# Kernel optimization log

Measured on AMD Instinct MI355X. Metric: run time of the kernel, lower is better.

The kernel has to match this reference:

```python
import jax, jax.numpy as jnp
import numpy as np

H = 64      # num query heads
HKV = 8     # num key/value heads
D = 64      # head_dim
HID = 2880  # hidden_size
B = 8       # batch (num sequences)
Q = 16      # query tokens per sequence
P = 128     # kv pages per sequence
PAGE = 16   # kv page size
NPAGES = 2048  # total pages in cache pool
NEG = -1e9  # finite stand-in for -inf mask (avoids inf arithmetic; exp underflows to 0 identically)


def setup_inputs() -> dict:
    key = jax.random.key(0)
    ks = jax.random.split(key, 6)
    n = B * Q
    S = P * PAGE
    hidden_states = jax.random.normal(ks[0], (n, HID), jnp.float32) * 0.02
    kv_cache_at_layer = jax.random.normal(ks[1], (NPAGES, 2, PAGE, HKV, D), jnp.float32)
    qkv_dim = D * (H + 2 * HKV)
    w_qkv = jax.random.normal(ks[2], (qkv_dim, HID), jnp.float32) * 0.02
    b_qkv = jnp.zeros((qkv_dim,), jnp.float32)
    w_o = jax.random.normal(ks[3], (HID, H * D), jnp.float32) * 0.02
    b_o = jnp.zeros((HID,), jnp.float32)
    sinks = jax.random.normal(ks[4], (H,), jnp.float32)
    qo_indptr = (jnp.arange(B + 1) * Q).astype(jnp.int32)
    kv_page_indptr = (jnp.arange(B + 1) * P).astype(jnp.int32)
    kv_last_page_lens = jnp.full((B,), PAGE, jnp.int32)
    kv_page_indices = jnp.asarray(np.random.default_rng(0).permutation(NPAGES)[:B * P], jnp.int32)
    # causal mask: query i of each sequence sits at absolute position S - Q + i
    qpos = S - Q + jnp.arange(Q)
    mask = jnp.where(jnp.arange(S)[None, :] <= qpos[:, None], 0.0, NEG).astype(jnp.float32)
    attention_mask = jnp.broadcast_to(mask[None], (B, Q, S)).reshape(-1)
    return dict(hidden_states=hidden_states, kv_cache_at_layer=kv_cache_at_layer,
                attention_mask=attention_mask, w_qkv=w_qkv, b_qkv=b_qkv, w_o=w_o, b_o=b_o,
                sinks=sinks, qo_indptr=qo_indptr, kv_page_indptr=kv_page_indptr,
                kv_last_page_lens=kv_last_page_lens, kv_page_indices=kv_page_indices)


def reference(hidden_states, kv_cache_at_layer, attention_mask, w_qkv, b_qkv, w_o, b_o,
              sinks, qo_indptr, kv_page_indptr, kv_last_page_lens, kv_page_indices):
    n = hidden_states.shape[0]
    b = qo_indptr.shape[0] - 1
    q_len = n // b                              # uniform ragged layout (see setup)
    p = kv_page_indices.shape[0] // b
    page = kv_cache_at_layer.shape[2]
    s = p * page
    g = H // HKV                                # query heads per kv head (GQA groups)
    scaling = D ** -0.5

    qkv = hidden_states @ w_qkv.T + b_qkv                       # [n, (H+2*HKV)*D]
    q = qkv[:, :H * D].reshape(b, q_len, HKV, g, D) * scaling    # [b q hkv g d]

    pages = kv_page_indices.reshape(b, p)
    k = kv_cache_at_layer[pages, 0].reshape(b, s, HKV, D)        # gather pages -> [b s hkv d]
    v = kv_cache_at_layer[pages, 1].reshape(b, s, HKV, D)

    scores = jnp.einsum('bqhgd,bshd->bhgqs', q, k).astype(jnp.float32)
    mask = attention_mask.reshape(b, q_len, s)
    # keys beyond the valid portion of the last page are invalid
    valid = jnp.arange(s)[None, :] < ((p - 1) * page + kv_last_page_lens[:, None])
    mask = jnp.where(valid[:, None, :], mask, NEG)
    scores = scores + mask[:, None, None, :, :]

    # online-softmax merge across pages is equivalent to this single pass;
    # running max starts at 0 in the original, hence the clamp to 0
    m = jnp.maximum(scores.max(axis=-1), 0.0)                    # [b hkv g q]
    pexp = jnp.exp(scores - m[..., None])                        # [b hkv g q s]
    sink = sinks.reshape(HKV, g).astype(jnp.float32)
    sum_exp = pexp.sum(axis=-1) + jnp.exp(sink[None, :, :, None] - m)
    num = jnp.einsum('bhgqs,bshd->bhgqd', pexp, v.astype(jnp.float32))
    attn = num / sum_exp[..., None]                              # [b hkv g q d]
    attn = attn.transpose(0, 3, 1, 2, 4).reshape(n, H * D)       # q (h d)
    return attn.astype(hidden_states.dtype) @ w_o.T + b_o
```

## Files before the change

### kernel.cpp

```cpp
#include <hip/hip_runtime.h>
#include <hip/hip_bf16.h>

#define BB      8
#define QL      16
#define NHKV    8
#define NG      8
#define DD      64
#define HIDN    2880
#define PP      128
#define PGSZ    16
#define SS      2048
#define NQ      4096
#define NSPLIT  8
#define KSQ     5
#define KCQ     576
#define KSO     8
#define KCO     512

typedef short bf16x8 __attribute__((ext_vector_type(8)));
typedef short short4v __attribute__((ext_vector_type(4)));
typedef float f32x4  __attribute__((ext_vector_type(4)));

__device__ inline short f2bf(float f) {
  __hip_bfloat16 h = __float2bfloat16(f);
  union { __hip_bfloat16 h; short s; } u; u.h = h;
  return u.s;
}

__device__ inline float bf2f(short s) {
  union { float f; unsigned u; } u;
  u.u = ((unsigned)(unsigned short)s) << 16;
  return u.f;
}

__device__ inline bf16x8 cvt8(float4 a, float4 b) {
  bf16x8 r;
  r[0] = f2bf(a.x); r[1] = f2bf(a.y); r[2] = f2bf(a.z); r[3] = f2bf(a.w);
  r[4] = f2bf(b.x); r[5] = f2bf(b.y); r[6] = f2bf(b.z); r[7] = f2bf(b.w);
  return r;
}

__device__ inline bf16x8 pack8(const float* __restrict__ p) {
  float4 a = *(const float4*)p;
  float4 b = *(const float4*)(p + 4);
  return cvt8(a, b);
}

__global__ __launch_bounds__(256) void k_qkv_split(const float* __restrict__ hid,
                                                   const float* __restrict__ wq,
                                                   short* __restrict__ qpart) {
  const int n0 = blockIdx.x * 32;
  const int ks = blockIdx.y;
  const int tid = threadIdx.x;
  const int wid = tid >> 6, lane = tid & 63;
  const int lo = lane & 15, hi = lane >> 4;
  const int m0 = wid * 32;

  const float* xr0 = hid + (size_t)(m0 + lo) * HIDN;
  const float* xr1 = hid + (size_t)(m0 + 16 + lo) * HIDN;
  const float* wr0 = wq + (size_t)(n0 + lo) * HIDN;
  const float* wr1 = wq + (size_t)(n0 + 16 + lo) * HIDN;
  const int kb = ks * KCQ + hi * 8;

  f32x4 acc[2][2];
#pragma unroll
  for (int mt = 0; mt < 2; ++mt)
#pragma unroll
    for (int nt = 0; nt < 2; ++nt) acc[mt][nt] = (f32x4){0.f, 0.f, 0.f, 0.f};

  float4 bufA[4][2], bufB[4][2];
#define LOADQ(dst, kk) { \
    dst[0][0] = *(const float4*)(xr0 + (kk)); dst[0][1] = *(const float4*)(xr0 + (kk) + 4); \
    dst[1][0] = *(const float4*)(xr1 + (kk)); dst[1][1] = *(const float4*)(xr1 + (kk) + 4); \
    dst[2][0] = *(const float4*)(wr0 + (kk)); dst[2][1] = *(const float4*)(wr0 + (kk) + 4); \
    dst[3][0] = *(const float4*)(wr1 + (kk)); dst[3][1] = *(const float4*)(wr1 + (kk) + 4); }
#define MFMAQ(buf) { \
    bf16x8 a0 = cvt8(buf[0][0], buf[0][1]); \
    bf16x8 a1 = cvt8(buf[1][0], buf[1][1]); \
    bf16x8 w0 = cvt8(buf[2][0], buf[2][1]); \
    bf16x8 w1 = cvt8(buf[3][0], buf[3][1]); \
    acc[0][0] = __builtin_amdgcn_mfma_f32_16x16x32_bf16(a0, w0, acc[0][0], 0, 0, 0); \
    acc[0][1] = __builtin_amdgcn_mfma_f32_16x16x32_bf16(a0, w1, acc[0][1], 0, 0, 0); \
    acc[1][0] = __builtin_amdgcn_mfma_f32_16x16x32_bf16(a1, w0, acc[1][0], 0, 0, 0); \
    acc[1][1] = __builtin_amdgcn_mfma_f32_16x16x32_bf16(a1, w1, acc[1][1], 0, 0, 0); }

  LOADQ(bufA, kb);
#pragma unroll
  for (int it = 0; it < 9; ++it) {
    const int kk = kb + it * 64;
    LOADQ(bufB, kk + 32);
    MFMAQ(bufA);
    if (it < 8) LOADQ(bufA, kk + 64);
    MFMAQ(bufB);
  }
#undef LOADQ
#undef MFMAQ

  short* qp = qpart + (size_t)ks * 128 * NQ;
#pragma unroll
  for (int mt = 0; mt < 2; ++mt)
#pragma unroll
    for (int nt = 0; nt < 2; ++nt)
#pragma unroll
      for (int r = 0; r < 4; ++r) {
        int m = m0 + mt * 16 + hi * 4 + r;
        int n = n0 + nt * 16 + lo;
        qp[(size_t)m * NQ + n] = f2bf(acc[mt][nt][r]);
      }
}

__global__ __launch_bounds__(256) void k_attn(const float* __restrict__ kvc,
                                              const int* __restrict__ pidx,
                                              const int* __restrict__ llen,
                                              const short* __restrict__ qpart,
                                              const float* __restrict__ bq,
                                              short* __restrict__ opart,
                                              float* __restrict__ lbuf) {
  const int blk = blockIdx.x;
  const int pair = blk >> 3, split = blk & 7;
  const int b = pair >> 3, kvh = pair & 7;
  const int tid = threadIdx.x;
  const int wid = tid >> 6, lane = tid & 63;
  const int lo = lane & 15, hi = lane >> 4;
  const int wrow = wid * 32;

  __shared__ short plds[128][72];
  __shared__ float vlds[64][65];

  bf16x8 qf[2][2];
#pragma unroll
  for (int mt = 0; mt < 2; ++mt) {
    int r = wrow + mt * 16 + lo;
    int g = r >> 4, qq = r & 15;
    int m = b * QL + qq;
    int h = kvh * NG + g;
#pragma unroll
    for (int kg = 0; kg < 2; ++kg) {
      int n = h * DD + kg * 32 + hi * 8;
      float4 bb0 = *(const float4*)(bq + n);
      float4 bb1 = *(const float4*)(bq + n + 4);
      float s[8];
      s[0] = bb0.x; s[1] = bb0.y; s[2] = bb0.z; s[3] = bb0.w;
      s[4] = bb1.x; s[5] = bb1.y; s[6] = bb1.z; s[7] = bb1.w;
#pragma unroll
      for (int k2 = 0; k2 < KSQ; ++k2) {
        bf16x8 p = *(const bf16x8*)(qpart + ((size_t)k2 * 128 + m) * NQ + n);
#pragma unroll
        for (int j = 0; j < 8; ++j) s[j] += bf2f(p[j]);
      }
      bf16x8 q8;
#pragma unroll
      for (int j = 0; j < 8; ++j) q8[j] = f2bf(s[j] * 0.125f);
      qf[mt][kg] = q8;
    }
  }

  float l_part[2][4];
  f32x4 o_acc[2][4];
#pragma unroll
  for (int mt = 0; mt < 2; ++mt)
#pragma unroll
    for (int j = 0; j < 4; ++j) l_part[mt][j] = 0.f;
#pragma unroll
  for (int mt = 0; mt < 2; ++mt)
#pragma unroll
    for (int dt = 0; dt < 4; ++dt) o_acc[mt][dt] = (f32x4){0.f, 0.f, 0.f, 0.f};

  const int sKeepEnd = (PP - 1) * PGSZ + llen[b];
  const int* pib = pidx + b * PP;
  const int sBeg = split * (SS / NSPLIT);
  const int sEnd = sBeg + (SS / NSPLIT);

  for (int s0 = sBeg; s0 < sEnd; s0 += 64) {
    const int p0 = s0 >> 4;

    float4 vreg[4];
    const int vsr = tid >> 4;
    const int vc4 = (tid & 15) * 4;
#pragma unroll
    for (int pc = 0; pc < 4; ++pc) {
      int pg = pib[p0 + pc];
      vreg[pc] = *(const float4*)(kvc +
          ((((size_t)pg * 2 + 1) * PGSZ + vsr) * NHKV + kvh) * DD + vc4);
    }

    f32x4 sc[2][4];
#pragma unroll
    for (int mt = 0; mt < 2; ++mt)
#pragma unroll
      for (int nt = 0; nt < 4; ++nt) sc[mt][nt] = (f32x4){0.f, 0.f, 0.f, 0.f};

#pragma unroll
    for (int nt = 0; nt < 4; ++nt) {
      int pg = pib[p0 + nt];
      const float* kp = kvc + ((((size_t)pg * 2 + 0) * PGSZ + lo) * NHKV + kvh) * DD;
#pragma unroll
      for (int kg = 0; kg < 2; ++kg) {
        bf16x8 kf = pack8(kp + kg * 32 + hi * 8);
        sc[0][nt] = __builtin_amdgcn_mfma_f32_16x16x32_bf16(qf[0][kg], kf, sc[0][nt], 0, 0, 0);
        sc[1][nt] = __builtin_amdgcn_mfma_f32_16x16x32_bf16(qf[1][kg], kf, sc[1][nt], 0, 0, 0);
      }
    }

    if (s0 + 64 > SS - QL) {
#pragma unroll
      for (int mt = 0; mt < 2; ++mt)
#pragma unroll
        for (int j = 0; j < 4; ++j) {
          int r = wrow + mt * 16 + hi * 4 + j;
          int qq = r & 15;
          int sLimQ = (SS - QL) + qq;
#pragma unroll
          for (int nt = 0; nt < 4; ++nt) {
            int s = s0 + nt * 16 + lo;
            bool keep = (s <= sLimQ) && (s < sKeepEnd);
            sc[mt][nt][j] = keep ? sc[mt][nt][j] : -1.0e9f;
          }
        }
    }

#pragma unroll
    for (int mt = 0; mt < 2; ++mt)
#pragma unroll
      for (int j = 0; j < 4; ++j)
#pragma unroll
        for (int nt = 0; nt < 4; ++nt) {
          float p = __expf(sc[mt][nt][j]);
          sc[mt][nt][j] = p;
          l_part[mt][j] += p;
        }

    __syncthreads();
#pragma unroll
    for (int pc = 0; pc < 4; ++pc) {
      int sl = pc * 16 + vsr;
      vlds[sl][vc4]     = vreg[pc].x;
      vlds[sl][vc4 + 1] = vreg[pc].y;
      vlds[sl][vc4 + 2] = vreg[pc].z;
      vlds[sl][vc4 + 3] = vreg[pc].w;
    }
#pragma unroll
    for (int mt = 0; mt < 2; ++mt)
#pragma unroll
      for (int j = 0; j < 4; ++j) {
        int r = wrow + mt * 16 + hi * 4 + j;
#pragma unroll
        for (int nt = 0; nt < 4; ++nt)
          plds[r][nt * 16 + lo] = f2bf(sc[mt][nt][j]);
      }
    __syncthreads();

#pragma unroll
    for (int kg = 0; kg < 2; ++kg) {
      bf16x8 pa[2];
      pa[0] = *(const bf16x8*)(&plds[wrow + lo][kg * 32 + hi * 8]);
      pa[1] = *(const bf16x8*)(&plds[wrow + 16 + lo][kg * 32 + hi * 8]);
#pragma unroll
      for (int dt = 0; dt < 4; ++dt) {
        bf16x8 vf;
#pragma unroll
        for (int j = 0; j < 8; ++j)
          vf[j] = f2bf(vlds[kg * 32 + hi * 8 + j][dt * 16 + lo]);
        o_acc[0][dt] = __builtin_amdgcn_mfma_f32_16x16x32_bf16(pa[0], vf, o_acc[0][dt], 0, 0, 0);
        o_acc[1][dt] = __builtin_amdgcn_mfma_f32_16x16x32_bf16(pa[1], vf, o_acc[1][dt], 0, 0, 0);
      }
    }
  }

#pragma unroll
  for (int mt = 0; mt < 2; ++mt)
#pragma unroll
    for (int j = 0; j < 4; ++j)
#pragma unroll
      for (int off = 1; off < 16; off <<= 1)
        l_part[mt][j] += __shfl_xor(l_part[mt][j], off, 64);

  short* op = opart + (size_t)(pair * NSPLIT + split) * 128 * DD;
#pragma unroll
  for (int mt = 0; mt < 2; ++mt)
#pragma unroll
    for (int dt = 0; dt < 4; ++dt)
#pragma unroll
      for (int j = 0; j < 4; ++j) {
        int r = wrow + mt * 16 + hi * 4 + j;
        op[r * DD + dt * 16 + lo] = f2bf(o_acc[mt][dt][j]);
      }
  if (lo == 0) {
#pragma unroll
    for (int mt = 0; mt < 2; ++mt)
#pragma unroll
      for (int j = 0; j < 4; ++j) {
        int r = wrow + mt * 16 + hi * 4 + j;
        lbuf[(size_t)(pair * NSPLIT + split) * 128 + r] = l_part[mt][j];
      }
  }
}

__global__ __launch_bounds__(256) void k_merge(const short* __restrict__ opart,
                                               const float* __restrict__ lbuf,
                                               const float* __restrict__ sinks,
                                               short* __restrict__ attnbf) {
  const int pair = blockIdx.x;
  const int b = pair >> 3, kvh = pair & 7;
  const int tid = threadIdx.x;

  __shared__ float Ls[128];
  if (tid < 128) {
    int r = tid, g = r >> 4;
    float L = __expf(sinks[kvh * NG + g]);
#pragma unroll
    for (int s2 = 0; s2 < NSPLIT; ++s2)
      L += lbuf[(size_t)(pair * NSPLIT + s2) * 128 + r];
    Ls[r] = L;
  }
  __syncthreads();

  for (int u = tid; u < 128 * 16; u += 256) {
    int r = u >> 4, c4 = (u & 15) * 4;
    float o0 = 0.f, o1 = 0.f, o2 = 0.f, o3 = 0.f;
#pragma unroll
    for (int s2 = 0; s2 < NSPLIT; ++s2) {
      short4v pv = *(const short4v*)(opart +
          ((size_t)(pair * NSPLIT + s2) * 128 + r) * DD + c4);
      o0 += bf2f(pv[0]); o1 += bf2f(pv[1]); o2 += bf2f(pv[2]); o3 += bf2f(pv[3]);
    }
    float inv = 1.0f / Ls[r];
    int g = r >> 4, qq = r & 15;
    int h = kvh * NG + g;
    short4v ov;
    ov[0] = f2bf(o0 * inv); ov[1] = f2bf(o1 * inv);
    ov[2] = f2bf(o2 * inv); ov[3] = f2bf(o3 * inv);
    *(short4v*)(attnbf + (size_t)(b * QL + qq) * NQ + h * DD + c4) = ov;
  }
}

__global__ __launch_bounds__(256) void k_out_split(const short* __restrict__ attnbf,
                                                   const float* __restrict__ wo,
                                                   short* __restrict__ outpart) {
  const int n0 = blockIdx.x * 32;
  const int ks = blockIdx.y;
  const int tid = threadIdx.x;
  const int wid = tid >> 6, lane = tid & 63;
  const int lo = lane & 15, hi = lane >> 4;
  const int m0 = wid * 32;

  const short* ar0 = attnbf + (size_t)(m0 + lo) * NQ;
  const short* ar1 = attnbf + (size_t)(m0 + 16 + lo) * NQ;
  const float* wr0 = wo + (size_t)(n0 + lo) * NQ;
  const float* wr1 = wo + (size_t)(n0 + 16 + lo) * NQ;
  const int kb = ks * KCO + hi * 8;

  f32x4 acc[2][2];
#pragma unroll
  for (int mt = 0; mt < 2; ++mt)
#pragma unroll
    for (int nt = 0; nt < 2; ++nt) acc[mt][nt] = (f32x4){0.f, 0.f, 0.f, 0.f};

  bf16x8 aA[2], aB[2];
  float4 wA[2][2], wB[2][2];
#define LOADO(adst, wdst, kk) { \
    adst[0] = *(const bf16x8*)(ar0 + (kk)); \
    adst[1] = *(const bf16x8*)(ar1 + (kk)); \
    wdst[0][0] = *(const float4*)(wr0 + (kk)); wdst[0][1] = *(const float4*)(wr0 + (kk) + 4); \
    wdst[1][0] = *(const float4*)(wr1 + (kk)); wdst[1][1] = *(const float4*)(wr1 + (kk) + 4); }
#define MFMAO(abuf, wbuf) { \
    bf16x8 ww0 = cvt8(wbuf[0][0], wbuf[0][1]); \
    bf16x8 ww1 = cvt8(wbuf[1][0], wbuf[1][1]); \
    acc[0][0] = __builtin_amdgcn_mfma_f32_16x16x32_bf16(abuf[0], ww0, acc[0][0], 0, 0, 0); \
    acc[0][1] = __builtin_amdgcn_mfma_f32_16x16x32_bf16(abuf[0], ww1, acc[0][1], 0, 0, 0); \
    acc[1][0] = __builtin_amdgcn_mfma_f32_16x16x32_bf16(abuf[1], ww0, acc[1][0], 0, 0, 0); \
    acc[1][1] = __builtin_amdgcn_mfma_f32_16x16x32_bf16(abuf[1], ww1, acc[1][1], 0, 0, 0); }

  LOADO(aA, wA, kb);
#pragma unroll
  for (int it = 0; it < 8; ++it) {
    const int kk = kb + it * 64;
    LOADO(aB, wB, kk + 32);
    MFMAO(aA, wA);
    if (it < 7) LOADO(aA, wA, kk + 64);
    MFMAO(aB, wB);
  }
#undef LOADO
#undef MFMAO

  short* op = outpart + (size_t)ks * 128 * HIDN;
#pragma unroll
  for (int mt = 0; mt < 2; ++mt)
#pragma unroll
    for (int nt = 0; nt < 2; ++nt)
#pragma unroll
      for (int r = 0; r < 4; ++r) {
        int m = m0 + mt * 16 + hi * 4 + r;
        int n = n0 + nt * 16 + lo;
        op[(size_t)m * HIDN + n] = f2bf(acc[mt][nt][r]);
      }
}

__global__ __launch_bounds__(256) void k_ored(const short* __restrict__ outpart,
                                              const float* __restrict__ bo,
                                              float* __restrict__ out) {
  int idx = blockIdx.x * 256 + threadIdx.x;
  int m = idx / 720;
  int n = (idx - m * 720) * 4;
  float4 v = *(const float4*)(bo + n);
#pragma unroll
  for (int ks = 0; ks < KSO; ++ks) {
    short4v p = *(const short4v*)(outpart + ((size_t)ks * 128 + m) * HIDN + n);
    v.x += bf2f(p[0]); v.y += bf2f(p[1]); v.z += bf2f(p[2]); v.w += bf2f(p[3]);
  }
  *(float4*)(out + (size_t)m * HIDN + n) = v;
}

extern "C" void kernel_launch(void* const* d_in, const int* in_sizes, int n_in,
                              void* d_out, int out_size, void* d_ws, size_t ws_size,
                              hipStream_t stream) {
  const float* hid   = (const float*)d_in[0];
  const float* kvc   = (const float*)d_in[1];
  const float* wq    = (const float*)d_in[3];
  const float* bq    = (const float*)d_in[4];
  const float* wo    = (const float*)d_in[5];
  const float* bo    = (const float*)d_in[6];
  const float* sinks = (const float*)d_in[7];
  const int* llen    = (const int*)d_in[10];
  const int* pidx    = (const int*)d_in[11];
  float* out = (float*)d_out;

  char* ws = (char*)d_ws;
  short* qpart   = (short*)(ws + 0);
  short* attnbf  = (short*)(ws + 5242880);
  short* opart   = (short*)(ws + 6291456);
  float* lbuf    = (float*)(ws + 14680064);
  short* outpart = (short*)(ws + 14942208);

  k_qkv_split<<<dim3(128, KSQ), dim3(256), 0, stream>>>(hid, wq, qpart);
  k_attn<<<dim3(BB * NHKV * NSPLIT), dim3(256), 0, stream>>>(kvc, pidx, llen, qpart, bq, opart, lbuf);
  k_merge<<<dim3(BB * NHKV), dim3(256), 0, stream>>>(opart, lbuf, sinks, attnbf);
  k_out_split<<<dim3(HIDN / 32, KSO), dim3(256), 0, stream>>>(attnbf, wo, outpart);
  k_ored<<<dim3(360), dim3(256), 0, stream>>>(outpart, bo, out);
}
```

Before: 128.7 us.

## Software-pipeline K/V page loads in attention and split merge across more blocks

The attention loop is fully unrolled into four tiles with double-buffered V registers and K registers. The next tile's K and V page loads are issued right after the current QK MFMAs, so global latency overlaps with softmax and PV work. Page indices are preloaded into registers, and barriers use explicit lgkmcnt waits so pending global loads are not drained. The merge kernel is split four ways over head-dim columns to launch more blocks, at the cost of each block recomputing the row sums and higher register pressure in attention.

Result: slower. 134.3 us (+4.4%).

```diff
diff --git a/kernel.cpp b/kernel.cpp
--- a/kernel.cpp
+++ b/kernel.cpp
@@ -40,12 +40,6 @@
   return r;
 }
 
-__device__ inline bf16x8 pack8(const float* __restrict__ p) {
-  float4 a = *(const float4*)p;
-  float4 b = *(const float4*)(p + 4);
-  return cvt8(a, b);
-}
-
 __global__ __launch_bounds__(256) void k_qkv_split(const float* __restrict__ hid,
                                                    const float* __restrict__ wq,
                                                    short* __restrict__ qpart) {
@@ -169,103 +163,123 @@
   const int sKeepEnd = (PP - 1) * PGSZ + llen[b];
   const int* pib = pidx + b * PP;
   const int sBeg = split * (SS / NSPLIT);
-  const int sEnd = sBeg + (SS / NSPLIT);
-
-  for (int s0 = sBeg; s0 < sEnd; s0 += 64) {
-    const int p0 = s0 >> 4;
-
-    float4 vreg[4];
-    const int vsr = tid >> 4;
-    const int vc4 = (tid & 15) * 4;
-#pragma unroll
-    for (int pc = 0; pc < 4; ++pc) {
-      int pg = pib[p0 + pc];
-      vreg[pc] = *(const float4*)(kvc +
-          ((((size_t)pg * 2 + 1) * PGSZ + vsr) * NHKV + kvh) * DD + vc4);
-    }
-
-    f32x4 sc[2][4];
-#pragma unroll
-    for (int mt = 0; mt < 2; ++mt)
-#pragma unroll
-      for (int nt = 0; nt < 4; ++nt) sc[mt][nt] = (f32x4){0.f, 0.f, 0.f, 0.f};
-
-#pragma unroll
-    for (int nt = 0; nt < 4; ++nt) {
-      int pg = pib[p0 + nt];
-      const float* kp = kvc + ((((size_t)pg * 2 + 0) * PGSZ + lo) * NHKV + kvh) * DD;
-#pragma unroll
-      for (int kg = 0; kg < 2; ++kg) {
-        bf16x8 kf = pack8(kp + kg * 32 + hi * 8);
-        sc[0][nt] = __builtin_amdgcn_mfma_f32_16x16x32_bf16(qf[0][kg], kf, sc[0][nt], 0, 0, 0);
-        sc[1][nt] = __builtin_amdgcn_mfma_f32_16x16x32_bf16(qf[1][kg], kf, sc[1][nt], 0, 0, 0);
-      }
-    }
-
-    if (s0 + 64 > SS - QL) {
-#pragma unroll
-      for (int mt = 0; mt < 2; ++mt)
-#pragma unroll
-        for (int j = 0; j < 4; ++j) {
-          int r = wrow + mt * 16 + hi * 4 + j;
-          int qq = r & 15;
-          int sLimQ = (SS - QL) + qq;
-#pragma unroll
-          for (int nt = 0; nt < 4; ++nt) {
-            int s = s0 + nt * 16 + lo;
-            bool keep = (s <= sLimQ) && (s < sKeepEnd);
-            sc[mt][nt][j] = keep ? sc[mt][nt][j] : -1.0e9f;
-          }
-        }
-    }
-
-#pragma unroll
-    for (int mt = 0; mt < 2; ++mt)
-#pragma unroll
-      for (int j = 0; j < 4; ++j)
-#pragma unroll
-        for (int nt = 0; nt < 4; ++nt) {
-          float p = __expf(sc[mt][nt][j]);
-          sc[mt][nt][j] = p;
-          l_part[mt][j] += p;
-        }
-
-    __syncthreads();
-#pragma unroll
-    for (int pc = 0; pc < 4; ++pc) {
-      int sl = pc * 16 + vsr;
-      vlds[sl][vc4]     = vreg[pc].x;
-      vlds[sl][vc4 + 1] = vreg[pc].y;
-      vlds[sl][vc4 + 2] = vreg[pc].z;
-      vlds[sl][vc4 + 3] = vreg[pc].w;
-    }
-#pragma unroll
-    for (int mt = 0; mt < 2; ++mt)
-#pragma unroll
-      for (int j = 0; j < 4; ++j) {
-        int r = wrow + mt * 16 + hi * 4 + j;
-#pragma unroll
-        for (int nt = 0; nt < 4; ++nt)
-          plds[r][nt * 16 + lo] = f2bf(sc[mt][nt][j]);
-      }
-    __syncthreads();
-
-#pragma unroll
-    for (int kg = 0; kg < 2; ++kg) {
-      bf16x8 pa[2];
-      pa[0] = *(const bf16x8*)(&plds[wrow + lo][kg * 32 + hi * 8]);
-      pa[1] = *(const bf16x8*)(&plds[wrow + 16 + lo][kg * 32 + hi * 8]);
-#pragma unroll
-      for (int dt = 0; dt < 4; ++dt) {
-        bf16x8 vf;
-#pragma unroll
-        for (int j = 0; j < 8; ++j)
-          vf[j] = f2bf(vlds[kg * 32 + hi * 8 + j][dt * 16 + lo]);
-        o_acc[0][dt] = __builtin_amdgcn_mfma_f32_16x16x32_bf16(pa[0], vf, o_acc[0][dt], 0, 0, 0);
-        o_acc[1][dt] = __builtin_amdgcn_mfma_f32_16x16x32_bf16(pa[1], vf, o_acc[1][dt], 0, 0, 0);
-      }
-    }
-  }
+
+  const int vsr = tid >> 4;
+  const int vc4 = (tid & 15) * 4;
+
+  int pga[16];
+#pragma unroll
+  for (int i = 0; i < 16; ++i) pga[i] = pib[(sBeg >> 4) + i];
+
+  float4 kreg[4][4];
+  float4 vregA[4], vregB[4];
+
+#define KLOAD(NT, PG) { \
+    const float* kp_ = kvc + ((((size_t)(PG) * 2 + 0) * PGSZ + lo) * NHKV + kvh) * DD + hi * 8; \
+    kreg[NT][0] = *(const float4*)(kp_);      kreg[NT][1] = *(const float4*)(kp_ + 4); \
+    kreg[NT][2] = *(const float4*)(kp_ + 32); kreg[NT][3] = *(const float4*)(kp_ + 36); }
+#define VLOAD(DST, PC, PG) { \
+    DST[PC] = *(const float4*)(kvc + ((((size_t)(PG) * 2 + 1) * PGSZ + vsr) * NHKV + kvh) * DD + vc4); }
+#define BARX() { asm volatile("s_waitcnt lgkmcnt(0)" ::: "memory"); \
+    __builtin_amdgcn_s_barrier(); __builtin_amdgcn_sched_barrier(0); }
+
+#pragma unroll
+  for (int nt = 0; nt < 4; ++nt) KLOAD(nt, pga[nt]);
+#pragma unroll
+  for (int pc = 0; pc < 4; ++pc) VLOAD(vregA, pc, pga[pc]);
+
+#define TILE(S0, PI, VCUR, VNXT, PRE) { \
+    f32x4 sc[2][4]; \
+    _Pragma("unroll") \
+    for (int nt = 0; nt < 4; ++nt) { \
+      sc[0][nt] = (f32x4){0.f, 0.f, 0.f, 0.f}; \
+      sc[1][nt] = (f32x4){0.f, 0.f, 0.f, 0.f}; \
+    } \
+    _Pragma("unroll") \
+    for (int nt = 0; nt < 4; ++nt) { \
+      bf16x8 kf0 = cvt8(kreg[nt][0], kreg[nt][1]); \
+      bf16x8 kf1 = cvt8(kreg[nt][2], kreg[nt][3]); \
+      sc[0][nt] = __builtin_amdgcn_mfma_f32_16x16x32_bf16(qf[0][0], kf0, sc[0][nt], 0, 0, 0); \
+      sc[1][nt] = __builtin_amdgcn_mfma_f32_16x16x32_bf16(qf[1][0], kf0, sc[1][nt], 0, 0, 0); \
+      sc[0][nt] = __builtin_amdgcn_mfma_f32_16x16x32_bf16(qf[0][1], kf1, sc[0][nt], 0, 0, 0); \
+      sc[1][nt] = __builtin_amdgcn_mfma_f32_16x16x32_bf16(qf[1][1], kf1, sc[1][nt], 0, 0, 0); \
+    } \
+    if (PRE) { \
+      _Pragma("unroll") \
+      for (int nt = 0; nt < 4; ++nt) KLOAD(nt, pga[(PI) + 4 + nt]); \
+      _Pragma("unroll") \
+      for (int pc = 0; pc < 4; ++pc) VLOAD(VNXT, pc, pga[(PI) + 4 + pc]); \
+    } \
+    if ((S0) + 64 > SS - QL) { \
+      _Pragma("unroll") \
+      for (int mt = 0; mt < 2; ++mt) \
+        _Pragma("unroll") \
+        for (int j = 0; j < 4; ++j) { \
+          int r = wrow + mt * 16 + hi * 4 + j; \
+          int qq = r & 15; \
+          int sLimQ = (SS - QL) + qq; \
+          _Pragma("unroll") \
+          for (int nt = 0; nt < 4; ++nt) { \
+            int s = (S0) + nt * 16 + lo; \
+            bool keep = (s <= sLimQ) && (s < sKeepEnd); \
+            sc[mt][nt][j] = keep ? sc[mt][nt][j] : -1.0e9f; \
+          } \
+        } \
+    } \
+    _Pragma("unroll") \
+    for (int mt = 0; mt < 2; ++mt) \
+      _Pragma("unroll") \
+      for (int j = 0; j < 4; ++j) \
+        _Pragma("unroll") \
+        for (int nt = 0; nt < 4; ++nt) { \
+          float p = __expf(sc[mt][nt][j]); \
+          sc[mt][nt][j] = p; \
+          l_part[mt][j] += p; \
+        } \
+    BARX(); \
+    _Pragma("unroll") \
+    for (int pc = 0; pc < 4; ++pc) { \
+      int sl = pc * 16 + vsr; \
+      vlds[sl][vc4]     = VCUR[pc].x; \
+      vlds[sl][vc4 + 1] = VCUR[pc].y; \
+      vlds[sl][vc4 + 2] = VCUR[pc].z; \
+      vlds[sl][vc4 + 3] = VCUR[pc].w; \
+    } \
+    _Pragma("unroll") \
+    for (int mt = 0; mt < 2; ++mt) \
+      _Pragma("unroll") \
+      for (int j = 0; j < 4; ++j) { \
+        int r = wrow + mt * 16 + hi * 4 + j; \
+        _Pragma("unroll") \
+        for (int nt = 0; nt < 4; ++nt) \
+          plds[r][nt * 16 + lo] = f2bf(sc[mt][nt][j]); \
+      } \
+    BARX(); \
+    _Pragma("unroll") \
+    for (int kg = 0; kg < 2; ++kg) { \
+      bf16x8 pa0 = *(const bf16x8*)(&plds[wrow + lo][kg * 32 + hi * 8]); \
+      bf16x8 pa1 = *(const bf16x8*)(&plds[wrow + 16 + lo][kg * 32 + hi * 8]); \
+      _Pragma("unroll") \
+      for (int dt = 0; dt < 4; ++dt) { \
+        bf16x8 vf; \
+        _Pragma("unroll") \
+        for (int j = 0; j < 8; ++j) \
+          vf[j] = f2bf(vlds[kg * 32 + hi * 8 + j][dt * 16 + lo]); \
+        o_acc[0][dt] = __builtin_amdgcn_mfma_f32_16x16x32_bf16(pa0, vf, o_acc[0][dt], 0, 0, 0); \
+        o_acc[1][dt] = __builtin_amdgcn_mfma_f32_16x16x32_bf16(pa1, vf, o_acc[1][dt], 0, 0, 0); \
+      } \
+    } \
+  }
+
+  TILE(sBeg,       0,  vregA, vregB, 1)
+  TILE(sBeg + 64,  4,  vregB, vregA, 1)
+  TILE(sBeg + 128, 8,  vregA, vregB, 1)
+  TILE(sBeg + 192, 12, vregB, vregA, 0)
+
+#undef TILE
+#undef BARX
+#undef KLOAD
+#undef VLOAD
 
 #pragma unroll
   for (int mt = 0; mt < 2; ++mt)
@@ -300,7 +314,7 @@
                                                const float* __restrict__ lbuf,
                                                const float* __restrict__ sinks,
                                                short* __restrict__ attnbf) {
-  const int pair = blockIdx.x;
+  const int pair = blockIdx.x >> 2, quarter = blockIdx.x & 3;
   const int b = pair >> 3, kvh = pair & 7;
   const int tid = threadIdx.x;
 
@@ -315,8 +329,8 @@
   }
   __syncthreads();
 
-  for (int u = tid; u < 128 * 16; u += 256) {
-    int r = u >> 4, c4 = (u & 15) * 4;
+  for (int u = tid; u < 128 * 4; u += 256) {
+    int r = u >> 2, c4 = (quarter * 4 + (u & 3)) * 4;
     float o0 = 0.f, o1 = 0.f, o2 = 0.f, o3 = 0.f;
 #pragma unroll
     for (int s2 = 0; s2 < NSPLIT; ++s2) {
@@ -434,7 +448,7 @@
 
   k_qkv_split<<<dim3(128, KSQ), dim3(256), 0, stream>>>(hid, wq, qpart);
   k_attn<<<dim3(BB * NHKV * NSPLIT), dim3(256), 0, stream>>>(kvc, pidx, llen, qpart, bq, opart, lbuf);
-  k_merge<<<dim3(BB * NHKV), dim3(256), 0, stream>>>(opart, lbuf, sinks, attnbf);
+  k_merge<<<dim3(BB * NHKV * 4), dim3(256), 0, stream>>>(opart, lbuf, sinks, attnbf);
   k_out_split<<<dim3(HIDN / 32, KSO), dim3(256), 0, stream>>>(attnbf, wo, outpart);
   k_ored<<<dim3(360), dim3(256), 0, stream>>>(outpart, bo, out);
 }
```

## Fuse split-KV merge into output projection GEMM A-fragment loads

Applied to the files above, without the earlier changes.

Removes the separate merge kernel and instead reduces the per-split partial outputs and normalizes them by the softmax denominator while building A fragments inside the output projection kernel. Each block recomputes inverse denominators for its kv head into shared memory. This drops one launch and the intermediate attn buffer write/read. In exchange, each of the 90 n-blocks redundantly reads and sums all 8 split partials, multiplying opart traffic roughly 90-fold (mostly from L2) and adding ALU work to the GEMM inner loop.

New measurement: 198.0 us. +53.9%, slower.

```diff
diff --git a/kernel.cpp b/kernel.cpp
--- a/kernel.cpp
+++ b/kernel.cpp
@@ -296,45 +296,9 @@
   }
 }
 
-__global__ __launch_bounds__(256) void k_merge(const short* __restrict__ opart,
-                                               const float* __restrict__ lbuf,
-                                               const float* __restrict__ sinks,
-                                               short* __restrict__ attnbf) {
-  const int pair = blockIdx.x;
-  const int b = pair >> 3, kvh = pair & 7;
-  const int tid = threadIdx.x;
-
-  __shared__ float Ls[128];
-  if (tid < 128) {
-    int r = tid, g = r >> 4;
-    float L = __expf(sinks[kvh * NG + g]);
-#pragma unroll
-    for (int s2 = 0; s2 < NSPLIT; ++s2)
-      L += lbuf[(size_t)(pair * NSPLIT + s2) * 128 + r];
-    Ls[r] = L;
-  }
-  __syncthreads();
-
-  for (int u = tid; u < 128 * 16; u += 256) {
-    int r = u >> 4, c4 = (u & 15) * 4;
-    float o0 = 0.f, o1 = 0.f, o2 = 0.f, o3 = 0.f;
-#pragma unroll
-    for (int s2 = 0; s2 < NSPLIT; ++s2) {
-      short4v pv = *(const short4v*)(opart +
-          ((size_t)(pair * NSPLIT + s2) * 128 + r) * DD + c4);
-      o0 += bf2f(pv[0]); o1 += bf2f(pv[1]); o2 += bf2f(pv[2]); o3 += bf2f(pv[3]);
-    }
-    float inv = 1.0f / Ls[r];
-    int g = r >> 4, qq = r & 15;
-    int h = kvh * NG + g;
-    short4v ov;
-    ov[0] = f2bf(o0 * inv); ov[1] = f2bf(o1 * inv);
-    ov[2] = f2bf(o2 * inv); ov[3] = f2bf(o3 * inv);
-    *(short4v*)(attnbf + (size_t)(b * QL + qq) * NQ + h * DD + c4) = ov;
-  }
-}
-
-__global__ __launch_bounds__(256) void k_out_split(const short* __restrict__ attnbf,
+__global__ __launch_bounds__(256) void k_out_fused(const short* __restrict__ opart,
+                                                   const float* __restrict__ lbuf,
+                                                   const float* __restrict__ sinks,
                                                    const float* __restrict__ wo,
                                                    short* __restrict__ outpart) {
   const int n0 = blockIdx.x * 32;
@@ -344,8 +308,20 @@
   const int lo = lane & 15, hi = lane >> 4;
   const int m0 = wid * 32;
 
-  const short* ar0 = attnbf + (size_t)(m0 + lo) * NQ;
-  const short* ar1 = attnbf + (size_t)(m0 + 16 + lo) * NQ;
+  __shared__ float invLs[8][128];
+  for (int u = tid; u < 8 * 128; u += 256) {
+    int b = u >> 7, r = u & 127;
+    int g = r >> 4;
+    float L = __expf(sinks[ks * NG + g]);
+#pragma unroll
+    for (int s2 = 0; s2 < NSPLIT; ++s2)
+      L += lbuf[(size_t)((b * NHKV + ks) * NSPLIT + s2) * 128 + r];
+    invLs[b][r] = 1.0f / L;
+  }
+  __syncthreads();
+
+  const int b0 = (m0 >> 4), b1 = b0 + 1;
+  const int qq = lo;
   const float* wr0 = wo + (size_t)(n0 + lo) * NQ;
   const float* wr1 = wo + (size_t)(n0 + 16 + lo) * NQ;
   const int kb = ks * KCO + hi * 8;
@@ -356,31 +332,49 @@
 #pragma unroll
     for (int nt = 0; nt < 2; ++nt) acc[mt][nt] = (f32x4){0.f, 0.f, 0.f, 0.f};
 
-  bf16x8 aA[2], aB[2];
   float4 wA[2][2], wB[2][2];
-#define LOADO(adst, wdst, kk) { \
-    adst[0] = *(const bf16x8*)(ar0 + (kk)); \
-    adst[1] = *(const bf16x8*)(ar1 + (kk)); \
+#define WLOAD(wdst, kk) { \
     wdst[0][0] = *(const float4*)(wr0 + (kk)); wdst[0][1] = *(const float4*)(wr0 + (kk) + 4); \
     wdst[1][0] = *(const float4*)(wr1 + (kk)); wdst[1][1] = *(const float4*)(wr1 + (kk) + 4); }
-#define MFMAO(abuf, wbuf) { \
+
+#define AFRAG(dst, B, kk) { \
+    int g_ = ((kk) >> 6) & 7; int d0_ = (kk) & 63; int rp_ = g_ * 16 + qq; \
+    const short* ob_ = opart + ((size_t)((B) * NHKV + ks) * NSPLIT * 8192) + rp_ * 64 + d0_; \
+    float s0_ = 0.f, s1_ = 0.f, s2_ = 0.f, s3_ = 0.f, s4_ = 0.f, s5_ = 0.f, s6_ = 0.f, s7_ = 0.f; \
+    _Pragma("unroll") \
+    for (int sp = 0; sp < NSPLIT; ++sp) { \
+      bf16x8 pv = *(const bf16x8*)(ob_ + sp * 8192); \
+      s0_ += bf2f(pv[0]); s1_ += bf2f(pv[1]); s2_ += bf2f(pv[2]); s3_ += bf2f(pv[3]); \
+      s4_ += bf2f(pv[4]); s5_ += bf2f(pv[5]); s6_ += bf2f(pv[6]); s7_ += bf2f(pv[7]); \
+    } \
+    float il_ = invLs[B][rp_]; \
+    dst[0] = f2bf(s0_ * il_); dst[1] = f2bf(s1_ * il_); \
+    dst[2] = f2bf(s2_ * il_); dst[3] = f2bf(s3_ * il_); \
+    dst[4] = f2bf(s4_ * il_); dst[5] = f2bf(s5_ * il_); \
+    dst[6] = f2bf(s6_ * il_); dst[7] = f2bf(s7_ * il_); }
+
+#define MFMAO(wbuf, kk) { \
+    bf16x8 a0, a1; \
+    AFRAG(a0, b0, kk); \
+    AFRAG(a1, b1, kk); \
     bf16x8 ww0 = cvt8(wbuf[0][0], wbuf[0][1]); \
     bf16x8 ww1 = cvt8(wbuf[1][0], wbuf[1][1]); \
-    acc[0][0] = __builtin_amdgcn_mfma_f32_16x16x32_bf16(abuf[0], ww0, acc[0][0], 0, 0, 0); \
-    acc[0][1] = __builtin_amdgcn_mfma_f32_16x16x32_bf16(abuf[0], ww1, acc[0][1], 0, 0, 0); \
-    acc[1][0] = __builtin_amdgcn_mfma_f32_16x16x32_bf16(abuf[1], ww0, acc[1][0], 0, 0, 0); \
-    acc[1][1] = __builtin_amdgcn_mfma_f32_16x16x32_bf16(abuf[1], ww1, acc[1][1], 0, 0, 0); }
-
-  LOADO(aA, wA, kb);
+    acc[0][0] = __builtin_amdgcn_mfma_f32_16x16x32_bf16(a0, ww0, acc[0][0], 0, 0, 0); \
+    acc[0][1] = __builtin_amdgcn_mfma_f32_16x16x32_bf16(a0, ww1, acc[0][1], 0, 0, 0); \
+    acc[1][0] = __builtin_amdgcn_mfma_f32_16x16x32_bf16(a1, ww0, acc[1][0], 0, 0, 0); \
+    acc[1][1] = __builtin_amdgcn_mfma_f32_16x16x32_bf16(a1, ww1, acc[1][1], 0, 0, 0); }
+
+  WLOAD(wA, kb);
 #pragma unroll
   for (int it = 0; it < 8; ++it) {
     const int kk = kb + it * 64;
-    LOADO(aB, wB, kk + 32);
-    MFMAO(aA, wA);
-    if (it < 7) LOADO(aA, wA, kk + 64);
-    MFMAO(aB, wB);
-  }
-#undef LOADO
+    WLOAD(wB, kk + 32);
+    MFMAO(wA, kk);
+    if (it < 7) WLOAD(wA, kk + 64);
+    MFMAO(wB, kk + 32);
+  }
+#undef WLOAD
+#undef AFRAG
 #undef MFMAO
 
   short* op = outpart + (size_t)ks * 128 * HIDN;
@@ -427,14 +421,12 @@
 
   char* ws = (char*)d_ws;
   short* qpart   = (short*)(ws + 0);
-  short* attnbf  = (short*)(ws + 5242880);
-  short* opart   = (short*)(ws + 6291456);
-  float* lbuf    = (float*)(ws + 14680064);
-  short* outpart = (short*)(ws + 14942208);
+  short* opart   = (short*)(ws + 5242880);
+  float* lbuf    = (float*)(ws + 13631488);
+  short* outpart = (short*)(ws + 13893632);
 
   k_qkv_split<<<dim3(128, KSQ), dim3(256), 0, stream>>>(hid, wq, qpart);
   k_attn<<<dim3(BB * NHKV * NSPLIT), dim3(256), 0, stream>>>(kvc, pidx, llen, qpart, bq, opart, lbuf);
-  k_merge<<<dim3(BB * NHKV), dim3(256), 0, stream>>>(opart, lbuf, sinks, attnbf);
-  k_out_split<<<dim3(HIDN / 32, KSO), dim3(256), 0, stream>>>(attnbf, wo, outpart);
+  k_out_fused<<<dim3(HIDN / 32, KSO), dim3(256), 0, stream>>>(opart, lbuf, sinks, wo, outpart);
   k_ored<<<dim3(360), dim3(256), 0, stream>>>(outpart, bo, out);
 }
```

## Increase split counts and add a separate Q-reduction kernel

Applied to the files above, without the earlier changes.

Doubles or triples the split-K and split-KV factors for the QKV GEMM, the attention, and the output GEMM, so each launch has more blocks and each block does less work. The Q partial-sum reduction and scaling moves out of the attention kernel into a new k_qred kernel that writes Q in the per-(batch, kv-head) layout the attention kernel reads directly. The merge kernel is split into quarters per pair to add more blocks. In exchange, the partial buffers are larger, there is more reduction traffic, and there is one extra kernel launch.

Result: slower. 136.6 us (+6.2%).

```diff
diff --git a/kernel.cpp b/kernel.cpp
--- a/kernel.cpp
+++ b/kernel.cpp
@@ -11,11 +11,11 @@
 #define PGSZ    16
 #define SS      2048
 #define NQ      4096
-#define NSPLIT  8
-#define KSQ     5
-#define KCQ     576
-#define KSO     8
-#define KCO     512
+#define NSPLIT  16
+#define KSQ     15
+#define KCQ     192
+#define KSO     16
+#define KCO     256
 
 typedef short bf16x8 __attribute__((ext_vector_type(8)));
 typedef short short4v __attribute__((ext_vector_type(4)));
@@ -86,11 +86,11 @@
 
   LOADQ(bufA, kb);
 #pragma unroll
-  for (int it = 0; it < 9; ++it) {
+  for (int it = 0; it < 3; ++it) {
     const int kk = kb + it * 64;
     LOADQ(bufB, kk + 32);
     MFMAQ(bufA);
-    if (it < 8) LOADQ(bufA, kk + 64);
+    if (it < 2) LOADQ(bufA, kk + 64);
     MFMAQ(bufB);
   }
 #undef LOADQ
@@ -109,15 +109,36 @@
       }
 }
 
+__global__ __launch_bounds__(256) void k_qred(const short* __restrict__ qpart,
+                                              const float* __restrict__ bq,
+                                              short* __restrict__ qbf) {
+  int idx = blockIdx.x * 256 + threadIdx.x;
+  int m = idx >> 10;
+  int n = (idx & 1023) * 4;
+  float4 bv = *(const float4*)(bq + n);
+  float s0 = bv.x, s1 = bv.y, s2 = bv.z, s3 = bv.w;
+#pragma unroll
+  for (int ks = 0; ks < KSQ; ++ks) {
+    short4v p = *(const short4v*)(qpart + ((size_t)ks * 128 + m) * NQ + n);
+    s0 += bf2f(p[0]); s1 += bf2f(p[1]); s2 += bf2f(p[2]); s3 += bf2f(p[3]);
+  }
+  int h = n >> 6, d = n & 63;
+  int kvh = h >> 3, g = h & 7;
+  int b = m >> 4, qq = m & 15;
+  short4v o;
+  o[0] = f2bf(s0 * 0.125f); o[1] = f2bf(s1 * 0.125f);
+  o[2] = f2bf(s2 * 0.125f); o[3] = f2bf(s3 * 0.125f);
+  *(short4v*)(qbf + ((size_t)((b * NHKV + kvh) * 128) + g * 16 + qq) * DD + d) = o;
+}
+
 __global__ __launch_bounds__(256) void k_attn(const float* __restrict__ kvc,
                                               const int* __restrict__ pidx,
                                               const int* __restrict__ llen,
-                                              const short* __restrict__ qpart,
-                                              const float* __restrict__ bq,
+                                              const short* __restrict__ qbf,
                                               short* __restrict__ opart,
                                               float* __restrict__ lbuf) {
   const int blk = blockIdx.x;
-  const int pair = blk >> 3, split = blk & 7;
+  const int pair = blk >> 4, split = blk & 15;
   const int b = pair >> 3, kvh = pair & 7;
   const int tid = threadIdx.x;
   const int wid = tid >> 6, lane = tid & 63;
@@ -128,32 +149,12 @@
   __shared__ float vlds[64][65];
 
   bf16x8 qf[2][2];
-#pragma unroll
-  for (int mt = 0; mt < 2; ++mt) {
-    int r = wrow + mt * 16 + lo;
-    int g = r >> 4, qq = r & 15;
-    int m = b * QL + qq;
-    int h = kvh * NG + g;
-#pragma unroll
-    for (int kg = 0; kg < 2; ++kg) {
-      int n = h * DD + kg * 32 + hi * 8;
-      float4 bb0 = *(const float4*)(bq + n);
-      float4 bb1 = *(const float4*)(bq + n + 4);
-      float s[8];
-      s[0] = bb0.x; s[1] = bb0.y; s[2] = bb0.z; s[3] = bb0.w;
-      s[4] = bb1.x; s[5] = bb1.y; s[6] = bb1.z; s[7] = bb1.w;
-#pragma unroll
-      for (int k2 = 0; k2 < KSQ; ++k2) {
-        bf16x8 p = *(const bf16x8*)(qpart + ((size_t)k2 * 128 + m) * NQ + n);
-#pragma unroll
-        for (int j = 0; j < 8; ++j) s[j] += bf2f(p[j]);
-      }
-      bf16x8 q8;
-#pragma unroll
-      for (int j = 0; j < 8; ++j) q8[j] = f2bf(s[j] * 0.125f);
-      qf[mt][kg] = q8;
-    }
-  }
+  const short* qp = qbf + (size_t)pair * 128 * DD;
+#pragma unroll
+  for (int mt = 0; mt < 2; ++mt)
+#pragma unroll
+    for (int kg = 0; kg < 2; ++kg)
+      qf[mt][kg] = *(const bf16x8*)(qp + (size_t)(wrow + mt * 16 + lo) * DD + kg * 32 + hi * 8);
 
   float l_part[2][4];
   f32x4 o_acc[2][4];
@@ -300,7 +301,7 @@
                                                const float* __restrict__ lbuf,
                                                const float* __restrict__ sinks,
                                                short* __restrict__ attnbf) {
-  const int pair = blockIdx.x;
+  const int pair = blockIdx.x >> 2, quarter = blockIdx.x & 3;
   const int b = pair >> 3, kvh = pair & 7;
   const int tid = threadIdx.x;
 
@@ -315,8 +316,8 @@
   }
   __syncthreads();
 
-  for (int u = tid; u < 128 * 16; u += 256) {
-    int r = u >> 4, c4 = (u & 15) * 4;
+  for (int u = tid; u < 128 * 4; u += 256) {
+    int r = u >> 2, c4 = (quarter * 4 + (u & 3)) * 4;
     float o0 = 0.f, o1 = 0.f, o2 = 0.f, o3 = 0.f;
 #pragma unroll
     for (int s2 = 0; s2 < NSPLIT; ++s2) {
@@ -373,11 +374,11 @@
 
   LOADO(aA, wA, kb);
 #pragma unroll
-  for (int it = 0; it < 8; ++it) {
+  for (int it = 0; it < 4; ++it) {
     const int kk = kb + it * 64;
     LOADO(aB, wB, kk + 32);
     MFMAO(aA, wA);
-    if (it < 7) LOADO(aA, wA, kk + 64);
+    if (it < 3) LOADO(aA, wA, kk + 64);
     MFMAO(aB, wB);
   }
 #undef LOADO
@@ -427,14 +428,16 @@
 
   char* ws = (char*)d_ws;
   short* qpart   = (short*)(ws + 0);
-  short* attnbf  = (short*)(ws + 5242880);
-  short* opart   = (short*)(ws + 6291456);
-  float* lbuf    = (float*)(ws + 14680064);
-  short* outpart = (short*)(ws + 14942208);
+  short* qbf     = (short*)(ws + 15728640);
+  short* opart   = (short*)(ws + 16777216);
+  float* lbuf    = (float*)(ws + 33554432);
+  short* attnbf  = (short*)(ws + 34078720);
+  short* outpart = (short*)(ws + 35127296);
 
   k_qkv_split<<<dim3(128, KSQ), dim3(256), 0, stream>>>(hid, wq, qpart);
-  k_attn<<<dim3(BB * NHKV * NSPLIT), dim3(256), 0, stream>>>(kvc, pidx, llen, qpart, bq, opart, lbuf);
-  k_merge<<<dim3(BB * NHKV), dim3(256), 0, stream>>>(opart, lbuf, sinks, attnbf);
+  k_qred<<<dim3(512), dim3(256), 0, stream>>>(qpart, bq, qbf);
+  k_attn<<<dim3(BB * NHKV * NSPLIT), dim3(256), 0, stream>>>(kvc, pidx, llen, qbf, opart, lbuf);
+  k_merge<<<dim3(BB * NHKV * 4), dim3(256), 0, stream>>>(opart, lbuf, sinks, attnbf);
   k_out_split<<<dim3(HIDN / 32, KSO), dim3(256), 0, stream>>>(attnbf, wo, outpart);
   k_ored<<<dim3(360), dim3(256), 0, stream>>>(outpart, bo, out);
 }
```
